# Optimization experiments

Measured on AMD Instinct MI355X. Metric: run time of the kernel, lower is better.

Reference implementation:

```python
import math
import jax, jax.numpy as jnp
import numpy as np

B, C, NX, NY = 8, 16, 512, 512
N = 16384
N_RES, NH, S = 90, 5, 0.5


def _normal(x, mu, s):
    # exp(-0.5*((x-mu)/s)^2) / (sqrt(s^2) * sqrt(2*pi))  -- matches torch helper
    return jnp.exp(-0.5 * ((x - mu) / s) ** 2) / (jnp.sqrt(s * s) * math.sqrt(2.0 * math.pi))


def setup_inputs() -> dict:
    key = jax.random.key(0)
    k1, k2 = jax.random.split(key)
    x = jax.random.normal(k1, (B, C, NX, NY), dtype=jnp.float32)
    coords = jax.random.uniform(k2, (B, N, 2), dtype=jnp.float32)
    nh_m = (NH - 1) / 2 + 0.5
    pixel_offset_normal = jnp.linspace(nh_m, -nh_m, N_RES, dtype=jnp.float32)
    pixel_offset_indices = jnp.linspace(-(NH - 1) // 2, (NH - 1) // 2, NH, dtype=jnp.float32)
    s = jnp.float32(S)
    return {"x": x, "coords": coords, "s": s,
            "pixel_offset_normal": pixel_offset_normal,
            "pixel_offset_indices": pixel_offset_indices}


def reference(x, coords, s, pixel_offset_normal, pixel_offset_indices):
    b, n, _ = coords.shape
    _, c, nx, ny = x.shape
    nh = pixel_offset_indices.shape[0]

    # continuous positions in pixel space
    px = coords[:, :, 1] * (nx - 1)   # [b,n]
    py = coords[:, :, 0] * (ny - 1)
    rpx, rpy = jnp.round(px), jnp.round(py)

    # gaussian weights integrated over sub-pixel resolution (n_res samples -> nh bins)
    # NOTE: torch code clamps both axes with x.shape[-2] (=nx); replicated faithfully.
    pxo = jnp.clip(rpx[..., None] - pixel_offset_normal, 0.0, nx)   # [b,n,n_res]
    pyo = jnp.clip(rpy[..., None] - pixel_offset_normal, 0.0, nx)
    wx = _normal(pxo, px[..., None], s).reshape(b, n, nh, -1).sum(-1)  # [b,n,nh]
    wy = _normal(pyo, py[..., None], s).reshape(b, n, nh, -1).sum(-1)
    w2d = wx[..., :, None] * wy[..., None, :]                          # [b,n,nh,nh]
    w2d = w2d / w2d.reshape(b, n, -1).sum(-1)[..., None, None]

    # integer neighborhood indices (both axes clamped with nx-1, as in torch code)
    ix = jnp.clip(jnp.round(rpx[..., None] - pixel_offset_indices), 0, nx - 1).astype(jnp.int32)  # [b,n,nh]
    iy = jnp.clip(jnp.round(rpy[..., None] - pixel_offset_indices), 0, nx - 1).astype(jnp.int32)

    # per-batch gather of nh x nh neighborhoods (equivalent to torch's BxB gather + diagonal)
    flat = (ix[..., :, None] * ny + iy[..., None, :]).reshape(b, n * nh * nh)  # [b, n*nh*nh]
    xf = x.reshape(b, c, nx * ny)
    g = jax.vmap(lambda xi, idx: xi[:, idx])(xf, flat)       # [b,c,n*nh*nh]
    g = g.reshape(b, c, n, nh, nh)

    out = (g * w2d[:, None]).reshape(b, c, n, nh * nh).sum(-1)  # [b,c,n]
    return out
```

## Files before the change

### kernel.cpp

```cpp
#include <hip/hip_runtime.h>

#define BV    8
#define CV    16
#define NXV   512
#define NYV   512
#define NV    16384
#define NRES  90
#define NHV   5
#define TPB   256

#define NPTS  (BV * NV)
#define TSH   5
#define TDIM  (NXV >> TSH)
#define NBUCKB (TDIM * TDIM)
#define NBUCK  (BV * NBUCKB)
#define SCANT 1024
#define SPT   (NBUCK / SCANT)

#define CPG   4
#define RROWS 36
#define RCOLS 48
#define RSEG  (RCOLS / 4)
#define SLOTS_PER_CH (RROWS * RSEG)
#define SLOTS (CPG * SLOTS_PER_CH)

#if __has_builtin(__builtin_amdgcn_exp2f)
#define EXP2 __builtin_amdgcn_exp2f
#else
#define EXP2 exp2f
#endif

__global__ void zero_counts_kernel(int* __restrict__ counts) {
    int i = blockIdx.x * blockDim.x + threadIdx.x;
    if (i < NBUCK) counts[i] = 0;
}

__device__ __forceinline__ int bucket_key(float rpx, float rpy, int i) {
    const int tr = ((int)rpx) >> TSH;
    const int tc = ((int)rpy) >> TSH;
    return (i >> 14) * NBUCKB + tr * TDIM + tc;
}

__global__ __launch_bounds__(TPB) void bucket_count_kernel(
    const float* __restrict__ coords, int* __restrict__ counts)
{
    const int i = blockIdx.x * TPB + threadIdx.x;
    const float2 cd = *(const float2*)(coords + (size_t)i * 2);
    const float rpx = rintf(cd.y * (float)(NXV - 1));
    const float rpy = rintf(cd.x * (float)(NYV - 1));
    atomicAdd(&counts[bucket_key(rpx, rpy, i)], 1);
}

__global__ __launch_bounds__(SCANT) void scan_kernel(
    const int* __restrict__ counts, int* __restrict__ starts,
    int* __restrict__ cursors)
{
    __shared__ int sm[SCANT];
    const int tid  = threadIdx.x;
    const int base = tid * SPT;

    int v[SPT];
    int run = 0;
    #pragma unroll
    for (int k = 0; k < SPT; ++k) {
        v[k] = run;
        run += counts[base + k];
    }
    sm[tid] = run;
    __syncthreads();
    #pragma unroll
    for (int off = 1; off < SCANT; off <<= 1) {
        int t = sm[tid];
        if (tid >= off) t += sm[tid - off];
        __syncthreads();
        sm[tid] = t;
        __syncthreads();
    }
    const int tbase = sm[tid] - run;
    #pragma unroll
    for (int k = 0; k < SPT; ++k) {
        const int e = tbase + v[k];
        starts[base + k]  = e;
        cursors[base + k] = e;
    }
}

__global__ __launch_bounds__(TPB) void scatter_weights_kernel(
    const float* __restrict__ coords,
    const float* __restrict__ s_ptr,
    const float* __restrict__ offn,
    const float* __restrict__ offi,
    int* __restrict__ cursors,
    float4* __restrict__ w8a, float4* __restrict__ w8b,
    float4* __restrict__ wx4, int4* __restrict__ off4,
    float4* __restrict__ misc)
{
    const int i = blockIdx.x * TPB + threadIdx.x;

    const float2 cd = *(const float2*)(coords + (size_t)i * 2);
    const float px  = cd.y * (float)(NXV - 1);
    const float py  = cd.x * (float)(NYV - 1);
    const float rpx = rintf(px);
    const float rpy = rintf(py);

    const int pos = atomicAdd(&cursors[bucket_key(rpx, rpy, i)], 1);

    const float s = s_ptr[0];
    const float k = -0.72134752044448169f / (s * s);

    float wx[NHV], wy[NHV];
    float sx = 0.f, sy = 0.f;
    #pragma unroll
    for (int h = 0; h < NHV; ++h) {
        float ax = 0.f, ay = 0.f;
        #pragma unroll 6
        for (int t = 0; t < NRES / NHV; ++t) {
            const float off = offn[h * (NRES / NHV) + t];
            const float vx = fminf(fmaxf(rpx - off, 0.f), (float)NXV);
            const float vy = fminf(fmaxf(rpy - off, 0.f), (float)NXV);
            const float dx = vx - px;
            const float dy = vy - py;
            ax += EXP2(k * dx * dx);
            ay += EXP2(k * dy * dy);
        }
        wx[h] = ax; wy[h] = ay;
        sx += ax;  sy += ay;
    }
    const float inv = 1.0f / (sx * sy);

    int ix[NHV], iy[NHV];
    #pragma unroll
    for (int h = 0; h < NHV; ++h) {
        const float fo = offi[h];
        ix[h] = (int)fminf(fmaxf(rintf(rpx - fo), 0.f), (float)(NXV - 1));
        iy[h] = (int)fminf(fmaxf(rintf(rpy - fo), 0.f), (float)(NXV - 1));
    }

    const int a = min(iy[NHV - 1] & ~3, NYV - 8);

    float w8[8];
    #pragma unroll
    for (int kk = 0; kk < 8; ++kk) {
        float w = 0.f;
        #pragma unroll
        for (int j = 0; j < NHV; ++j)
            w += (iy[j] - a == kk) ? wy[j] * inv : 0.f;
        w8[kk] = w;
    }

    w8a[pos] = make_float4(w8[0], w8[1], w8[2], w8[3]);
    w8b[pos] = make_float4(w8[4], w8[5], w8[6], w8[7]);
    wx4[pos] = make_float4(wx[0], wx[1], wx[2], wx[3]);
    off4[pos] = make_int4((ix[0] * NYV + a) * 4, (ix[1] * NYV + a) * 4,
                          (ix[2] * NYV + a) * 4, (ix[3] * NYV + a) * 4);
    misc[pos] = make_float4(wx[4], __int_as_float((ix[4] * NYV + a) * 4),
                            __int_as_float(i), 0.f);
}

__global__ __launch_bounds__(TPB) void tile_gather_kernel(
    const float* __restrict__ x,
    const int* __restrict__ starts, const int* __restrict__ ends,
    const float4* __restrict__ w8a, const float4* __restrict__ w8b,
    const float4* __restrict__ wx4, const int4* __restrict__ off4,
    const float4* __restrict__ misc,
    float* __restrict__ out)
{
    __shared__ float4 lds[SLOTS];

    const int bid = blockIdx.x;
    const int cg  = blockIdx.y;
    const int b   = bid >> 8;
    const int tr  = (bid >> 4) & (TDIM - 1);
    const int tc  = bid & (TDIM - 1);
    const int r0  = tr << TSH, c0 = tc << TSH;
    const int R0  = min(max(r0 - 2, 0), NXV - RROWS);
    const int W0  = min(max(c0 - 8, 0), NYV - RCOLS);

    const int tid = threadIdx.x;
    const char* bx = (const char*)x + ((size_t)(b * CV + cg * CPG) << 20);

    #pragma unroll
    for (int kk = 0; kk < (SLOTS + TPB - 1) / TPB; ++kk) {
        const int sslot = tid + kk * TPB;
        if (sslot < SLOTS) {
            const int ch  = sslot / SLOTS_PER_CH;
            const int rem = sslot - ch * SLOTS_PER_CH;
            const int row = rem / RSEG;
            const int seg = rem - row * RSEG;
            lds[sslot] = *(const float4*)(bx + ((size_t)ch << 20)
                          + ((size_t)(R0 + row) << 11) + (W0 << 2) + (seg << 4));
        }
    }
    __syncthreads();

    const int s0    = starts[bid];
    const int total = (ends[bid] - s0) << 2;
    const char* ldsb = (const char*)lds;

    for (int item = tid; item < total; item += TPB) {
        const int p  = s0 + (item >> 2);
        const int ch = item & (CPG - 1);

        const float4 wa = w8a[p];
        const float4 wb = w8b[p];
        const float4 wr = wx4[p];
        const int4   o4 = off4[p];
        const float4 ms = misc[p];
        const float  we = ms.x;
        const int    oe = __float_as_int(ms.y);
        const int    i  = __float_as_int(ms.z);
        const int    n  = i & (NV - 1);

        const int basech = ch * (SLOTS_PER_CH * 16) - R0 * (RCOLS * 4) - (W0 << 2);

        float acc = 0.f;
#define ROW(OFF, WROW) {                                                     \
        const int lo = basech + ((OFF) >> 11) * (RCOLS * 4) + ((OFF) & 2047);\
        const float4 va = *(const float4*)(ldsb + lo);                       \
        const float4 vb = *(const float4*)(ldsb + lo + 16);                  \
        const float rs = va.x * wa.x + va.y * wa.y + va.z * wa.z +           \
                         va.w * wa.w + vb.x * wb.x + vb.y * wb.y +           \
                         vb.z * wb.z + vb.w * wb.w;                          \
        acc = fmaf(WROW, rs, acc); }

        ROW(o4.x, wr.x)
        ROW(o4.y, wr.y)
        ROW(o4.z, wr.z)
        ROW(o4.w, wr.w)
        ROW(oe,   we)
#undef ROW

        out[(((size_t)(b * CV + cg * CPG + ch)) << 14) + n] = acc;
    }
}

extern "C" void kernel_launch(void* const* d_in, const int* in_sizes, int n_in,
                              void* d_out, int out_size, void* d_ws, size_t ws_size,
                              hipStream_t stream) {
    const float* x      = (const float*)d_in[0];
    const float* coords = (const float*)d_in[1];
    const float* s_ptr  = (const float*)d_in[2];
    const float* offn   = (const float*)d_in[3];
    const float* offi   = (const float*)d_in[4];
    float* out = (float*)d_out;

    char* w = (char*)d_ws;
    float4* w8a  = (float4*)w;  w += (size_t)NPTS * 16;
    float4* w8b  = (float4*)w;  w += (size_t)NPTS * 16;
    float4* wx4  = (float4*)w;  w += (size_t)NPTS * 16;
    int4*   off4 = (int4*)w;    w += (size_t)NPTS * 16;
    float4* misc = (float4*)w;  w += (size_t)NPTS * 16;
    int*    counts  = (int*)w;  w += (size_t)NBUCK * 4;
    int*    starts  = (int*)w;  w += (size_t)NBUCK * 4;
    int*    cursors = (int*)w;

    zero_counts_kernel<<<dim3(NBUCK / TPB), dim3(TPB), 0, stream>>>(counts);
    bucket_count_kernel<<<dim3(NPTS / TPB), dim3(TPB), 0, stream>>>(coords, counts);
    scan_kernel<<<dim3(1), dim3(SCANT), 0, stream>>>(counts, starts, cursors);
    scatter_weights_kernel<<<dim3(NPTS / TPB), dim3(TPB), 0, stream>>>(
        coords, s_ptr, offn, offi, cursors, w8a, w8b, wx4, off4, misc);

    dim3 grid(NBUCK, CV / CPG, 1);
    tile_gather_kernel<<<grid, dim3(TPB), 0, stream>>>(
        x, starts, cursors, w8a, w8b, wx4, off4, misc, out);
}
```

Before: 262.2 us.

## Enlarge spatial buckets, pad LDS rows, write sorted-order output then transpose

```diff
diff --git a/kernel.cpp b/kernel.cpp
--- a/kernel.cpp
+++ b/kernel.cpp
@@ -10,19 +10,21 @@
 #define TPB   256
 
 #define NPTS  (BV * NV)
-#define TSH   5
+#define TSH   6
 #define TDIM  (NXV >> TSH)
 #define NBUCKB (TDIM * TDIM)
 #define NBUCK  (BV * NBUCKB)
-#define SCANT 1024
-#define SPT   (NBUCK / SCANT)
-
-#define CPG   4
-#define RROWS 36
-#define RCOLS 48
+
+#define CPG   2
+#define NCG   (CV / CPG)
+#define RROWS 68
+#define RCOLS 72
 #define RSEG  (RCOLS / 4)
-#define SLOTS_PER_CH (RROWS * RSEG)
+#define SEGP  19
+#define SLOTS_PER_CH (RROWS * SEGP)
 #define SLOTS (CPG * SLOTS_PER_CH)
+#define CHB   (SLOTS_PER_CH * 16)
+#define ROWB  (SEGP * 16)
 
 #if __has_builtin(__builtin_amdgcn_exp2f)
 #define EXP2 __builtin_amdgcn_exp2f
@@ -31,8 +33,7 @@
 #endif
 
 __global__ void zero_counts_kernel(int* __restrict__ counts) {
-    int i = blockIdx.x * blockDim.x + threadIdx.x;
-    if (i < NBUCK) counts[i] = 0;
+    counts[threadIdx.x] = 0;
 }
 
 __device__ __forceinline__ int bucket_key(float rpx, float rpy, int i) {
@@ -51,38 +52,26 @@
     atomicAdd(&counts[bucket_key(rpx, rpy, i)], 1);
 }
 
-__global__ __launch_bounds__(SCANT) void scan_kernel(
+__global__ __launch_bounds__(NBUCK) void scan_kernel(
     const int* __restrict__ counts, int* __restrict__ starts,
     int* __restrict__ cursors)
 {
-    __shared__ int sm[SCANT];
-    const int tid  = threadIdx.x;
-    const int base = tid * SPT;
-
-    int v[SPT];
-    int run = 0;
-    #pragma unroll
-    for (int k = 0; k < SPT; ++k) {
-        v[k] = run;
-        run += counts[base + k];
-    }
-    sm[tid] = run;
+    __shared__ int sm[NBUCK];
+    const int tid = threadIdx.x;
+    const int v = counts[tid];
+    sm[tid] = v;
     __syncthreads();
     #pragma unroll
-    for (int off = 1; off < SCANT; off <<= 1) {
+    for (int off = 1; off < NBUCK; off <<= 1) {
         int t = sm[tid];
         if (tid >= off) t += sm[tid - off];
         __syncthreads();
         sm[tid] = t;
         __syncthreads();
     }
-    const int tbase = sm[tid] - run;
-    #pragma unroll
-    for (int k = 0; k < SPT; ++k) {
-        const int e = tbase + v[k];
-        starts[base + k]  = e;
-        cursors[base + k] = e;
-    }
+    const int e = sm[tid] - v;
+    starts[tid]  = e;
+    cursors[tid] = e;
 }
 
 __global__ __launch_bounds__(TPB) void scatter_weights_kernel(
@@ -93,7 +82,7 @@
     int* __restrict__ cursors,
     float4* __restrict__ w8a, float4* __restrict__ w8b,
     float4* __restrict__ wx4, int4* __restrict__ off4,
-    float4* __restrict__ misc)
+    float4* __restrict__ misc, int* __restrict__ posOf)
 {
     const int i = blockIdx.x * TPB + threadIdx.x;
 
@@ -104,6 +93,7 @@
     const float rpy = rintf(py);
 
     const int pos = atomicAdd(&cursors[bucket_key(rpx, rpy, i)], 1);
+    posOf[i] = pos;
 
     const float s = s_ptr[0];
     const float k = -0.72134752044448169f / (s * s);
@@ -154,7 +144,7 @@
     off4[pos] = make_int4((ix[0] * NYV + a) * 4, (ix[1] * NYV + a) * 4,
                           (ix[2] * NYV + a) * 4, (ix[3] * NYV + a) * 4);
     misc[pos] = make_float4(wx[4], __int_as_float((ix[4] * NYV + a) * 4),
-                            __int_as_float(i), 0.f);
+                            0.f, 0.f);
 }
 
 __global__ __launch_bounds__(TPB) void tile_gather_kernel(
@@ -163,43 +153,41 @@
     const float4* __restrict__ w8a, const float4* __restrict__ w8b,
     const float4* __restrict__ wx4, const int4* __restrict__ off4,
     const float4* __restrict__ misc,
-    float* __restrict__ out)
+    float* __restrict__ tmp)
 {
     __shared__ float4 lds[SLOTS];
 
     const int bid = blockIdx.x;
     const int cg  = blockIdx.y;
-    const int b   = bid >> 8;
-    const int tr  = (bid >> 4) & (TDIM - 1);
+    const int b   = bid >> 6;
+    const int tr  = (bid >> 3) & (TDIM - 1);
     const int tc  = bid & (TDIM - 1);
     const int r0  = tr << TSH, c0 = tc << TSH;
     const int R0  = min(max(r0 - 2, 0), NXV - RROWS);
-    const int W0  = min(max(c0 - 8, 0), NYV - RCOLS);
+    const int W0  = min(max(c0 - 4, 0), NYV - RCOLS);
 
     const int tid = threadIdx.x;
     const char* bx = (const char*)x + ((size_t)(b * CV + cg * CPG) << 20);
 
-    #pragma unroll
-    for (int kk = 0; kk < (SLOTS + TPB - 1) / TPB; ++kk) {
-        const int sslot = tid + kk * TPB;
-        if (sslot < SLOTS) {
-            const int ch  = sslot / SLOTS_PER_CH;
-            const int rem = sslot - ch * SLOTS_PER_CH;
-            const int row = rem / RSEG;
-            const int seg = rem - row * RSEG;
+    for (int sslot = tid; sslot < SLOTS; sslot += TPB) {
+        const int ch  = sslot / SLOTS_PER_CH;
+        const int rem = sslot - ch * SLOTS_PER_CH;
+        const int row = rem / SEGP;
+        const int seg = rem - row * SEGP;
+        if (seg < RSEG)
             lds[sslot] = *(const float4*)(bx + ((size_t)ch << 20)
                           + ((size_t)(R0 + row) << 11) + (W0 << 2) + (seg << 4));
-        }
     }
     __syncthreads();
 
     const int s0    = starts[bid];
-    const int total = (ends[bid] - s0) << 2;
+    const int total = (ends[bid] - s0) << 1;
     const char* ldsb = (const char*)lds;
+    float* tout = tmp + (size_t)cg * (NPTS * CPG);
 
     for (int item = tid; item < total; item += TPB) {
-        const int p  = s0 + (item >> 2);
-        const int ch = item & (CPG - 1);
+        const int p   = s0 + (item >> 1);
+        const int chl = item & (CPG - 1);
 
         const float4 wa = w8a[p];
         const float4 wb = w8b[p];
@@ -208,14 +196,12 @@
         const float4 ms = misc[p];
         const float  we = ms.x;
         const int    oe = __float_as_int(ms.y);
-        const int    i  = __float_as_int(ms.z);
-        const int    n  = i & (NV - 1);
-
-        const int basech = ch * (SLOTS_PER_CH * 16) - R0 * (RCOLS * 4) - (W0 << 2);
+
+        const int basech = chl * CHB - R0 * ROWB - (W0 << 2);
 
         float acc = 0.f;
 #define ROW(OFF, WROW) {                                                     \
-        const int lo = basech + ((OFF) >> 11) * (RCOLS * 4) + ((OFF) & 2047);\
+        const int lo = basech + ((OFF) >> 11) * ROWB + ((OFF) & 2047);       \
         const float4 va = *(const float4*)(ldsb + lo);                       \
         const float4 vb = *(const float4*)(ldsb + lo + 16);                  \
         const float rs = va.x * wa.x + va.y * wa.y + va.z * wa.z +           \
@@ -230,8 +216,20 @@
         ROW(oe,   we)
 #undef ROW
 
-        out[(((size_t)(b * CV + cg * CPG + ch)) << 14) + n] = acc;
-    }
+        tout[(size_t)p * CPG + chl] = acc;
+    }
+}
+
+__global__ __launch_bounds__(TPB) void transpose_kernel(
+    const float* __restrict__ tmp, const int* __restrict__ posOf,
+    float* __restrict__ out)
+{
+    const int idx = blockIdx.x * TPB + threadIdx.x;
+    const int n = idx & (NV - 1);
+    const int c = (idx >> 14) & (CV - 1);
+    const int b = idx >> 18;
+    const int p = posOf[(b << 14) | n];
+    out[idx] = tmp[(size_t)(c >> 1) * (NPTS * CPG) + (size_t)p * CPG + (c & 1)];
 }
 
 extern "C" void kernel_launch(void* const* d_in, const int* in_sizes, int n_in,
@@ -250,17 +248,22 @@
     float4* wx4  = (float4*)w;  w += (size_t)NPTS * 16;
     int4*   off4 = (int4*)w;    w += (size_t)NPTS * 16;
     float4* misc = (float4*)w;  w += (size_t)NPTS * 16;
+    float*  tmp  = (float*)w;   w += (size_t)NPTS * CV * 4;
+    int*    posOf = (int*)w;    w += (size_t)NPTS * 4;
     int*    counts  = (int*)w;  w += (size_t)NBUCK * 4;
     int*    starts  = (int*)w;  w += (size_t)NBUCK * 4;
     int*    cursors = (int*)w;
 
-    zero_counts_kernel<<<dim3(NBUCK / TPB), dim3(TPB), 0, stream>>>(counts);
+    zero_counts_kernel<<<dim3(1), dim3(NBUCK), 0, stream>>>(counts);
     bucket_count_kernel<<<dim3(NPTS / TPB), dim3(TPB), 0, stream>>>(coords, counts);
-    scan_kernel<<<dim3(1), dim3(SCANT), 0, stream>>>(counts, starts, cursors);
+    scan_kernel<<<dim3(1), dim3(NBUCK), 0, stream>>>(counts, starts, cursors);
     scatter_weights_kernel<<<dim3(NPTS / TPB), dim3(TPB), 0, stream>>>(
-        coords, s_ptr, offn, offi, cursors, w8a, w8b, wx4, off4, misc);
-
-    dim3 grid(NBUCK, CV / CPG, 1);
+        coords, s_ptr, offn, offi, cursors, w8a, w8b, wx4, off4, misc, posOf);
+
+    dim3 grid(NBUCK, NCG, 1);
     tile_gather_kernel<<<grid, dim3(TPB), 0, stream>>>(
-        x, starts, cursors, w8a, w8b, wx4, off4, misc, out);
-}
+        x, starts, cursors, w8a, w8b, wx4, off4, misc, tmp);
+
+    transpose_kernel<<<dim3(NPTS * CV / TPB), dim3(TPB), 0, stream>>>(
+        tmp, posOf, out);
+}
```

Result: slower. 312.9 us (+19.4%).
